# Kernel tuning notes

Hardware: AMD Instinct MI355X
Metric: run time of the kernel (lower is better)

Reference implementation:

```python
import jax, jax.numpy as jnp
import numpy as np

T, B = 256, 512
IMG_FLAT = 25          # 5*5*num_channels
FEAT = 16; LOC = 4; EMB = 4
LSTM_IN = FEAT + LOC + EMB  # 24
H = 128
GRID = 10.0


def _lin(k, out_d, in_d, scale=0.05):
    kw, kb = jax.random.split(k)
    return (jax.random.normal(kw, (out_d, in_d), jnp.float32) * scale,
            jax.random.normal(kb, (out_d,), jnp.float32) * scale)


def setup_inputs() -> dict:
    key = jax.random.key(0)
    ks = jax.random.split(key, 16)
    image = jax.random.uniform(ks[0], (T * B, 5, 5), jnp.float32) * 255.0
    location = jax.random.uniform(ks[1], (T * B, 2), jnp.float32) * GRID
    message = jax.random.normal(ks[2], (T * B, 1), jnp.float32)
    done = jax.random.randint(ks[3], (T * B,), 0, 2, jnp.int32)
    h0 = jnp.zeros((1, B, H), jnp.float32)
    c0 = jnp.zeros((1, B, H), jnp.float32)
    Wv1, bv1 = _lin(ks[4], 256, IMG_FLAT)
    Wv2, bv2 = _lin(ks[5], 256, 256)
    Wv3, bv3 = _lin(ks[6], 128, 256)
    Wv4, bv4 = _lin(ks[7], FEAT, 128)
    Wl, bl = _lin(ks[8], LOC, 2)
    Wm, bm = _lin(ks[9], EMB, 1)
    Wih, bih = _lin(ks[10], 4 * H, LSTM_IN)
    Whh, bhh = _lin(ks[11], 4 * H, H)
    return dict(image=image, location=location, message=message, done=done,
                h0=h0, c0=c0,
                Wv1=Wv1, bv1=bv1, Wv2=Wv2, bv2=bv2, Wv3=Wv3, bv3=bv3,
                Wv4=Wv4, bv4=bv4, Wl=Wl, bl=bl, Wm=Wm, bm=bm,
                Wih=Wih, bih=bih, Whh=Whh, bhh=bhh)


def _get_states(image, location, message, done_f, h0, c0,
                Wv1, bv1, Wv2, bv2, Wv3, bv3, Wv4, bv4,
                Wl, bl, Wm, bm, Wih, bih, Whh, bhh):
    batch = h0.shape[1]
    # encoders (all rows at once, faithful to torch version)
    x = image.reshape(image.shape[0], -1) / 255.0
    f = jax.nn.relu(x @ Wv1.T + bv1)
    f = jax.nn.relu(f @ Wv2.T + bv2)
    f = jax.nn.relu(f @ Wv3.T + bv3)
    image_feat = jax.nn.relu(f @ Wv4.T + bv4)                  # [TB, 16]
    loc_feat = (location / GRID) @ Wl.T + bl                    # [TB, 4]
    msg = (1.0 - done_f)[:, None] * message
    msg_feat = jax.nn.relu(msg @ Wm.T + bm)                     # [TB, 4]
    hid = jnp.concatenate([image_feat, loc_feat, msg_feat], axis=1)
    hid = hid.reshape(-1, batch, LSTM_IN)                       # [T, B, 24]
    d_seq = done_f.reshape(-1, batch)                           # [T, B]

    def step(carry, xd):
        h, c = carry
        x_t, d_t = xd
        mask = (1.0 - d_t)[:, None]
        h = h * mask
        c = c * mask
        gates = x_t @ Wih.T + bih + h @ Whh.T + bhh             # [B, 4H]
        i, fg, g, o = jnp.split(gates, 4, axis=-1)
        c = jax.nn.sigmoid(fg) * c + jax.nn.sigmoid(i) * jnp.tanh(g)
        h = jax.nn.sigmoid(o) * jnp.tanh(c)
        return (h, c), h

    (hT, cT), hs = jax.lax.scan(step, (h0[0], c0[0]), (hid, d_seq))
    new_hidden = hs.reshape(-1, H)                              # [TB, 128]
    return new_hidden, hT[None], cT[None]


def reference(image, location, message, done, h0, c0,
              Wv1, bv1, Wv2, bv2, Wv3, bv3, Wv4, bv4,
              Wl, bl, Wm, bm, Wih, bih, Whh, bhh):
    done_f = done.astype(jnp.float32)
    return _get_states(image, location, message, done_f, h0, c0,
                       Wv1, bv1, Wv2, bv2, Wv3, bv3, Wv4, bv4,
                       Wl, bl, Wm, bm, Wih, bih, Whh, bhh)
```

## Files before the change

kernel.cpp:

```cpp
#include <hip/hip_runtime.h>
#include <hip/hip_bf16.h>

#define T_STEPS 256
#define BATCH   512
#define HID     128
#define TBROWS  (T_STEPS * BATCH)
#define XH_STRIDE 32

typedef short  bh8   __attribute__((ext_vector_type(8)));
typedef _Float16 h8  __attribute__((ext_vector_type(8)));
typedef float  f32x4 __attribute__((ext_vector_type(4)));

__device__ __forceinline__ unsigned short f2bf_bits(float x) {
    union { float f; unsigned int u; } a; a.f = x;
    unsigned int r = a.u + 0x7fffu + ((a.u >> 16) & 1u);
    return (unsigned short)(r >> 16);
}
__device__ __forceinline__ unsigned short f2h_bits(float x) {
    union { _Float16 h; unsigned short u; } z; z.h = (_Float16)x; return z.u;
}
__device__ __forceinline__ unsigned int pack2h(float a, float b) {
    union { _Float16 h[2]; unsigned int u; } z;
    z.h[0] = (_Float16)a; z.h[1] = (_Float16)b; return z.u;
}
__device__ __forceinline__ unsigned int pack2bf(float a, float b) {
    return (unsigned int)f2bf_bits(a) | ((unsigned int)f2bf_bits(b) << 16);
}

#if __has_builtin(__builtin_amdgcn_rcpf)
__device__ __forceinline__ float frcp(float x) { return __builtin_amdgcn_rcpf(x); }
#else
__device__ __forceinline__ float frcp(float x) { return 1.0f / x; }
#endif
#if __has_builtin(__builtin_amdgcn_exp2f)
__device__ __forceinline__ float fexp2(float x) { return __builtin_amdgcn_exp2f(x); }
#else
__device__ __forceinline__ float fexp2(float x) { return __expf(x * 0.6931471806f); }
#endif
#define LOG2E 1.442695041f
__device__ __forceinline__ float sigf(float x) {
    return frcp(1.0f + fexp2(-x * LOG2E));
}
__device__ __forceinline__ float tanh_fast(float x) {
    return fmaf(-2.0f, frcp(1.0f + fexp2(x * (2.0f * LOG2E))), 1.0f);
}

__device__ __forceinline__ float swz16(float v) {
    return __int_as_float(
        __builtin_amdgcn_ds_swizzle(__float_as_int(v), 0x000F));
}

__device__ __forceinline__ void barrier_lds_only() {
    asm volatile("s_waitcnt lgkmcnt(0)" ::: "memory");
    __builtin_amdgcn_s_barrier();
    asm volatile("" ::: "memory");
}

__device__ __forceinline__ void fragstore(unsigned short* dst, const float* W,
                                          int i, int NT, int Kreal) {
    const int j    = i & 7;
    const int lane = (i >> 3) & 63;
    const int ts   = i >> 9;
    const int nt   = ts % NT;
    const int ks   = ts / NT;
    const int n = nt * 16 + (lane & 15);
    const int k = ks * 32 + (lane >> 4) * 8 + j;
    dst[i] = (k < Kreal) ? f2bf_bits(W[n * Kreal + k]) : (unsigned short)0;
}

#define NE1 8192
#define NE2 65536
#define NE3 32768
#define NE4 2048
#define NWC 81920
#define NBS 512
#define PREP_TOTAL (NE1 + NE2 + NE3 + NE4 + NWC + NBS)

__global__ __launch_bounds__(256) void prep_kernel(
    const float* __restrict__ W1, const float* __restrict__ W2,
    const float* __restrict__ W3, const float* __restrict__ W4,
    const float* __restrict__ Wih, const float* __restrict__ bih,
    const float* __restrict__ Whh, const float* __restrict__ bhh,
    unsigned short* __restrict__ w1f, unsigned short* __restrict__ w2f,
    unsigned short* __restrict__ w3f, unsigned short* __restrict__ w4f,
    unsigned short* __restrict__ wcf, float* __restrict__ bsum)
{
    int i = blockIdx.x * 256 + threadIdx.x;
    if (i < NE1) { fragstore(w1f, W1, i, 16, 25); return; }
    i -= NE1;
    if (i < NE2) { fragstore(w2f, W2, i, 16, 256); return; }
    i -= NE2;
    if (i < NE3) { fragstore(w3f, W3, i, 8, 256); return; }
    i -= NE3;
    if (i < NE4) { fragstore(w4f, W4, i, 1, 128); return; }
    i -= NE4;
    if (i < NWC) {
        const int j    = i & 7;
        const int lane = (i >> 3) & 63;
        const int ts   = i >> 9;
        const int mt   = ts / 5;
        const int kt   = ts - mt * 5;
        const int m = mt * 16 + (lane & 15);
        const int k = kt * 32 + (lane >> 4) * 8 + j;
        float v = 0.0f;
        if (k < 128)      v = Whh[m * 128 + k];
        else if (k < 152) v = Wih[m * 24 + (k - 128)];
        wcf[i] = f2h_bits(v);
        return;
    }
    i -= NWC;
    if (i < NBS) bsum[i] = bih[i] + bhh[i];
}

#define ASTRIDE 264

__global__ __launch_bounds__(256) void encoder_kernel(
    const float* __restrict__ img,
    const float* __restrict__ loc,
    const float* __restrict__ msg,
    const int*   __restrict__ done,
    const float* __restrict__ B1, const float* __restrict__ B2,
    const float* __restrict__ B3, const float* __restrict__ B4,
    const float* __restrict__ Wl, const float* __restrict__ Bl,
    const float* __restrict__ Wm, const float* __restrict__ Bm,
    const unsigned short* __restrict__ w1f, const unsigned short* __restrict__ w2f,
    const unsigned short* __restrict__ w3f, const unsigned short* __restrict__ w4f,
    unsigned short* __restrict__ xcat_h)
{
    __shared__ __align__(16) unsigned short actA[4][32][ASTRIDE];
    __shared__ __align__(16) unsigned short actB[4][32][ASTRIDE];

    const int tid  = threadIdx.x;
    const int w    = tid >> 6;
    const int lane = tid & 63;
    const int n    = lane & 15;
    const int quad = lane >> 4;
    const int wrow0 = blockIdx.x * 128 + w * 32;

    if (tid < 128) {
        const int grow = blockIdx.x * 128 + tid;
        const float l0 = loc[(size_t)grow * 2 + 0] * 0.1f;
        const float l1 = loc[(size_t)grow * 2 + 1] * 0.1f;
        #pragma unroll
        for (int c = 0; c < 4; ++c)
            xcat_h[(size_t)grow * XH_STRIDE + 16 + c] =
                f2h_bits(fmaf(Wl[c * 2 + 0], l0, fmaf(Wl[c * 2 + 1], l1, Bl[c])));
        const float mm = (1.0f - (float)done[grow]) * msg[grow];
        #pragma unroll
        for (int c = 0; c < 4; ++c)
            xcat_h[(size_t)grow * XH_STRIDE + 20 + c] =
                f2h_bits(fmaxf(fmaf(Wm[c], mm, Bm[c]), 0.0f));
    }

    const f32x4 zero4 = {0.0f, 0.0f, 0.0f, 0.0f};

    {
        bh8 bimg[2];
        #pragma unroll
        for (int sg = 0; sg < 2; ++sg) {
            const size_t grow = wrow0 + sg * 16 + n;
            #pragma unroll
            for (int j = 0; j < 8; ++j) {
                const int k = quad * 8 + j;
                const float v = (k < 25) ? img[grow * 25 + k] * (1.0f / 255.0f) : 0.0f;
                bimg[sg][j] = (short)f2bf_bits(v);
            }
        }
        f32x4 a1[16][2];
        #pragma unroll
        for (int mt = 0; mt < 16; ++mt) {
            const bh8 a = *reinterpret_cast<const bh8*>(w1f + (size_t)(mt * 64 + lane) * 8);
            a1[mt][0] = __builtin_amdgcn_mfma_f32_16x16x32_bf16(a, bimg[0], zero4, 0, 0, 0);
            a1[mt][1] = __builtin_amdgcn_mfma_f32_16x16x32_bf16(a, bimg[1], zero4, 0, 0, 0);
        }
        #pragma unroll
        for (int mt = 0; mt < 16; ++mt) {
            const float4 bv = *reinterpret_cast<const float4*>(B1 + mt * 16 + quad * 4);
            #pragma unroll
            for (int sg = 0; sg < 2; ++sg) {
                const float v0 = fmaxf(a1[mt][sg][0] + bv.x, 0.0f);
                const float v1 = fmaxf(a1[mt][sg][1] + bv.y, 0.0f);
                const float v2 = fmaxf(a1[mt][sg][2] + bv.z, 0.0f);
                const float v3 = fmaxf(a1[mt][sg][3] + bv.w, 0.0f);
                uint2 pk; pk.x = pack2bf(v0, v1); pk.y = pack2bf(v2, v3);
                *reinterpret_cast<uint2*>(&actA[w][sg * 16 + n][mt * 16 + quad * 4]) = pk;
            }
        }
    }
    __syncthreads();

    {
        f32x4 a2[16][2];
        #pragma unroll
        for (int mt = 0; mt < 16; ++mt) { a2[mt][0] = zero4; a2[mt][1] = zero4; }
        #pragma unroll
        for (int kt = 0; kt < 8; ++kt) {
            const bh8 b0 = *reinterpret_cast<const bh8*>(&actA[w][n][kt * 32 + quad * 8]);
            const bh8 b1 = *reinterpret_cast<const bh8*>(&actA[w][16 + n][kt * 32 + quad * 8]);
            #pragma unroll
            for (int mt = 0; mt < 16; ++mt) {
                const bh8 a = *reinterpret_cast<const bh8*>(
                    w2f + (size_t)((kt * 16 + mt) * 64 + lane) * 8);
                a2[mt][0] = __builtin_amdgcn_mfma_f32_16x16x32_bf16(a, b0, a2[mt][0], 0, 0, 0);
                a2[mt][1] = __builtin_amdgcn_mfma_f32_16x16x32_bf16(a, b1, a2[mt][1], 0, 0, 0);
            }
        }
        #pragma unroll
        for (int mt = 0; mt < 16; ++mt) {
            const float4 bv = *reinterpret_cast<const float4*>(B2 + mt * 16 + quad * 4);
            #pragma unroll
            for (int sg = 0; sg < 2; ++sg) {
                const float v0 = fmaxf(a2[mt][sg][0] + bv.x, 0.0f);
                const float v1 = fmaxf(a2[mt][sg][1] + bv.y, 0.0f);
                const float v2 = fmaxf(a2[mt][sg][2] + bv.z, 0.0f);
                const float v3 = fmaxf(a2[mt][sg][3] + bv.w, 0.0f);
                uint2 pk; pk.x = pack2bf(v0, v1); pk.y = pack2bf(v2, v3);
                *reinterpret_cast<uint2*>(&actB[w][sg * 16 + n][mt * 16 + quad * 4]) = pk;
            }
        }
    }
    __syncthreads();

    {
        f32x4 a3[8][2];
        #pragma unroll
        for (int mt = 0; mt < 8; ++mt) { a3[mt][0] = zero4; a3[mt][1] = zero4; }
        #pragma unroll
        for (int kt = 0; kt < 8; ++kt) {
            const bh8 b0 = *reinterpret_cast<const bh8*>(&actB[w][n][kt * 32 + quad * 8]);
            const bh8 b1 = *reinterpret_cast<const bh8*>(&actB[w][16 + n][kt * 32 + quad * 8]);
            #pragma unroll
            for (int mt = 0; mt < 8; ++mt) {
                const bh8 a = *reinterpret_cast<const bh8*>(
                    w3f + (size_t)((kt * 8 + mt) * 64 + lane) * 8);
                a3[mt][0] = __builtin_amdgcn_mfma_f32_16x16x32_bf16(a, b0, a3[mt][0], 0, 0, 0);
                a3[mt][1] = __builtin_amdgcn_mfma_f32_16x16x32_bf16(a, b1, a3[mt][1], 0, 0, 0);
            }
        }
        #pragma unroll
        for (int mt = 0; mt < 8; ++mt) {
            const float4 bv = *reinterpret_cast<const float4*>(B3 + mt * 16 + quad * 4);
            #pragma unroll
            for (int sg = 0; sg < 2; ++sg) {
                const float v0 = fmaxf(a3[mt][sg][0] + bv.x, 0.0f);
                const float v1 = fmaxf(a3[mt][sg][1] + bv.y, 0.0f);
                const float v2 = fmaxf(a3[mt][sg][2] + bv.z, 0.0f);
                const float v3 = fmaxf(a3[mt][sg][3] + bv.w, 0.0f);
                uint2 pk; pk.x = pack2bf(v0, v1); pk.y = pack2bf(v2, v3);
                *reinterpret_cast<uint2*>(&actA[w][sg * 16 + n][mt * 16 + quad * 4]) = pk;
            }
        }
    }
    __syncthreads();

    {
        f32x4 a4[2] = {zero4, zero4};
        #pragma unroll
        for (int kt = 0; kt < 4; ++kt) {
            const bh8 b0 = *reinterpret_cast<const bh8*>(&actA[w][n][kt * 32 + quad * 8]);
            const bh8 b1 = *reinterpret_cast<const bh8*>(&actA[w][16 + n][kt * 32 + quad * 8]);
            const bh8 a = *reinterpret_cast<const bh8*>(w4f + (size_t)(kt * 64 + lane) * 8);
            a4[0] = __builtin_amdgcn_mfma_f32_16x16x32_bf16(a, b0, a4[0], 0, 0, 0);
            a4[1] = __builtin_amdgcn_mfma_f32_16x16x32_bf16(a, b1, a4[1], 0, 0, 0);
        }
        const float4 bv = *reinterpret_cast<const float4*>(B4 + quad * 4);
        #pragma unroll
        for (int sg = 0; sg < 2; ++sg) {
            const int grow = wrow0 + sg * 16 + n;
            const float v0 = fmaxf(a4[sg][0] + bv.x, 0.0f);
            const float v1 = fmaxf(a4[sg][1] + bv.y, 0.0f);
            const float v2 = fmaxf(a4[sg][2] + bv.z, 0.0f);
            const float v3 = fmaxf(a4[sg][3] + bv.w, 0.0f);
            uint2 pk; pk.x = pack2h(v0, v1); pk.y = pack2h(v2, v3);
            *reinterpret_cast<uint2*>(xcat_h + (size_t)grow * XH_STRIDE + quad * 4) = pk;
        }
    }
}

#define COLS 2

__global__ __launch_bounds__(512) void lstm_kernel(
    const unsigned short* __restrict__ xcat_h,
    const int*   __restrict__ done,
    const float* __restrict__ h0,
    const float* __restrict__ c0,
    const unsigned short* __restrict__ wcf,
    const float* __restrict__ bsum,
    float* __restrict__ out)
{
    __shared__ __align__(16) unsigned short xls[T_STEPS][COLS][32];
    __shared__ __align__(16) unsigned short hx[2][COLS][HID];
    __shared__ int dls[T_STEPS][COLS];

    const int tid  = threadIdx.x;
    const int w    = tid >> 6;
    const int lane = tid & 63;
    const int n    = lane & 15;
    const int quad = lane >> 4;
    const int bb   = blockIdx.x * COLS;

    for (int i = tid; i < T_STEPS * COLS * 16; i += 512) {
        const int dw = i & 15;
        const int rc = i >> 4;
        const int st = rc >> 1, cl = rc & 1;
        unsigned int v = 0u;
        if (dw < 12)
            v = *reinterpret_cast<const unsigned int*>(
                xcat_h + (size_t)(st * BATCH + bb + cl) * XH_STRIDE + dw * 2);
        *reinterpret_cast<unsigned int*>(&xls[st][cl][dw * 2]) = v;
    }
    if (tid < T_STEPS * COLS) {
        const int st = tid >> 1, cl = tid & 1;
        dls[st][cl] = done[st * BATCH + bb + cl];
    }

    h8 wf[4][5];
    #pragma unroll
    for (int g = 0; g < 4; ++g)
        #pragma unroll
        for (int kt = 0; kt < 5; ++kt)
            wf[g][kt] = *reinterpret_cast<const h8*>(
                wcf + (size_t)(((g * 8 + w) * 5 + kt) * 64 + lane) * 8);

    const int unit = w * 16 + n;
    f32x4 bini[4];
    #pragma unroll
    for (int g = 0; g < 4; ++g) {
        const float b = bsum[g * 128 + unit];
        bini[g] = (f32x4){b, b, b, b};
    }

    const bool owner = (lane < 32);
    const int col = quad & 1;

    float c_ = 0.0f, h0v = 0.0f;
    if (owner) {
        c_  = c0[(size_t)(bb + col) * HID + unit];
        h0v = h0[(size_t)(bb + col) * HID + unit];
    }
    __syncthreads();

    if (owner)
        hx[0][col][unit] = f2h_bits(h0v * (1.0f - (float)dls[0][col]));
    __syncthreads();

    float hl = 0.0f;

    h8 bf[5];
    #pragma unroll
    for (int kt = 0; kt < 5; ++kt) bf[kt] = (h8)(_Float16)0.0f;

    #pragma unroll 1
    for (int s = 0; s < T_STEPS; ++s) {
        const int buf = s & 1;

        if (n < COLS) {
            #pragma unroll
            for (int kt = 0; kt < 4; ++kt)
                bf[kt] = *reinterpret_cast<const h8*>(&hx[buf][n][kt * 32 + quad * 8]);
            bf[4] = *reinterpret_cast<const h8*>(&xls[s][n][quad * 8]);
        }

        const int sn = (s + 1 < T_STEPS) ? s + 1 : T_STEPS - 1;
        const int m_cur = dls[s][col];
        const int m_nxt = dls[sn][col];

        f32x4 acc[4];
        #pragma unroll
        for (int g = 0; g < 4; ++g) acc[g] = bini[g];
        #pragma unroll
        for (int kt = 0; kt < 5; ++kt)
            #pragma unroll
            for (int g = 0; g < 4; ++g)
                acc[g] = __builtin_amdgcn_mfma_f32_16x16x32_f16(
                    bf[kt], wf[g][kt], acc[g], 0, 0, 0);

        float g4[4];
        #pragma unroll
        for (int g = 0; g < 4; ++g) {
            const float t0 = swz16(acc[g][0]);
            const float t1 = swz16(acc[g][1]);
            g4[g] = (lane & 16) ? t1 : t0;
        }

        if (owner) {
            const float cn = sigf(g4[1]) * (c_ * (1.0f - (float)m_cur))
                           + sigf(g4[0]) * tanh_fast(g4[2]);
            const float hn = sigf(g4[3]) * tanh_fast(cn);
            c_ = cn; hl = hn;
            out[(size_t)(s * BATCH + bb + col) * HID + unit] = hn;
            hx[buf ^ 1][col][unit] = f2h_bits(hn * (1.0f - (float)m_nxt));
        }
        barrier_lds_only();
    }

    const size_t base = (size_t)TBROWS * HID;
    if (owner) {
        out[base + (size_t)(bb + col) * HID + unit] = hl;
        out[base + (size_t)BATCH * HID + (size_t)(bb + col) * HID + unit] = c_;
    }
}

extern "C" void kernel_launch(void* const* d_in, const int* in_sizes, int n_in,
                              void* d_out, int out_size, void* d_ws, size_t ws_size,
                              hipStream_t stream) {
    const float* img  = (const float*)d_in[0];
    const float* loc  = (const float*)d_in[1];
    const float* msg  = (const float*)d_in[2];
    const int*   done = (const int*)d_in[3];
    const float* h0   = (const float*)d_in[4];
    const float* c0   = (const float*)d_in[5];
    const float* W1   = (const float*)d_in[6];
    const float* B1   = (const float*)d_in[7];
    const float* W2   = (const float*)d_in[8];
    const float* B2   = (const float*)d_in[9];
    const float* W3   = (const float*)d_in[10];
    const float* B3   = (const float*)d_in[11];
    const float* W4   = (const float*)d_in[12];
    const float* B4   = (const float*)d_in[13];
    const float* Wl   = (const float*)d_in[14];
    const float* Bl   = (const float*)d_in[15];
    const float* Wm   = (const float*)d_in[16];
    const float* Bm   = (const float*)d_in[17];
    const float* Wih  = (const float*)d_in[18];
    const float* bih  = (const float*)d_in[19];
    const float* Whh  = (const float*)d_in[20];
    const float* bhh  = (const float*)d_in[21];

    char* wsb = (char*)d_ws;
    unsigned short* xcat_h = (unsigned short*)wsb;
    unsigned short* w1f = (unsigned short*)(wsb + (size_t)TBROWS * XH_STRIDE * 2);
    unsigned short* w2f = w1f + NE1;
    unsigned short* w3f = w2f + NE2;
    unsigned short* w4f = w3f + NE3;
    unsigned short* wcf = w4f + NE4;
    float*          bsum = (float*)(wcf + NWC);

    float* out = (float*)d_out;

    prep_kernel<<<(PREP_TOTAL + 255) / 256, 256, 0, stream>>>(
        W1, W2, W3, W4, Wih, bih, Whh, bhh,
        w1f, w2f, w3f, w4f, wcf, bsum);
    encoder_kernel<<<TBROWS / 128, 256, 0, stream>>>(
        img, loc, msg, done, B1, B2, B3, B4, Wl, Bl, Wm, Bm,
        w1f, w2f, w3f, w4f, xcat_h);
    lstm_kernel<<<BATCH / COLS, 512, 0, stream>>>(
        xcat_h, done, h0, c0, wcf, bsum, out);
}
```

Before: 378.1 us.

## Assign one batch column per LSTM block and drop cross-lane swizzle

```diff
diff --git a/kernel.cpp b/kernel.cpp
--- a/kernel.cpp
+++ b/kernel.cpp
@@ -43,11 +43,6 @@
 }
 __device__ __forceinline__ float tanh_fast(float x) {
     return fmaf(-2.0f, frcp(1.0f + fexp2(x * (2.0f * LOG2E))), 1.0f);
-}
-
-__device__ __forceinline__ float swz16(float v) {
-    return __int_as_float(
-        __builtin_amdgcn_ds_swizzle(__float_as_int(v), 0x000F));
 }
 
 __device__ __forceinline__ void barrier_lds_only() {
@@ -277,9 +272,7 @@
     }
 }
 
-#define COLS 2
-
-__global__ __launch_bounds__(512) void lstm_kernel(
+__global__ __launch_bounds__(512, 4) void lstm_kernel(
     const unsigned short* __restrict__ xcat_h,
     const int*   __restrict__ done,
     const float* __restrict__ h0,
@@ -288,31 +281,27 @@
     const float* __restrict__ bsum,
     float* __restrict__ out)
 {
-    __shared__ __align__(16) unsigned short xls[T_STEPS][COLS][32];
-    __shared__ __align__(16) unsigned short hx[2][COLS][HID];
-    __shared__ int dls[T_STEPS][COLS];
+    __shared__ __align__(16) unsigned short xls[T_STEPS][32];
+    __shared__ __align__(16) unsigned short hx[2][HID];
+    __shared__ int dls[T_STEPS];
 
     const int tid  = threadIdx.x;
     const int w    = tid >> 6;
     const int lane = tid & 63;
     const int n    = lane & 15;
     const int quad = lane >> 4;
-    const int bb   = blockIdx.x * COLS;
-
-    for (int i = tid; i < T_STEPS * COLS * 16; i += 512) {
+    const int b    = blockIdx.x;
+
+    for (int i = tid; i < T_STEPS * 16; i += 512) {
         const int dw = i & 15;
-        const int rc = i >> 4;
-        const int st = rc >> 1, cl = rc & 1;
+        const int st = i >> 4;
         unsigned int v = 0u;
         if (dw < 12)
             v = *reinterpret_cast<const unsigned int*>(
-                xcat_h + (size_t)(st * BATCH + bb + cl) * XH_STRIDE + dw * 2);
-        *reinterpret_cast<unsigned int*>(&xls[st][cl][dw * 2]) = v;
-    }
-    if (tid < T_STEPS * COLS) {
-        const int st = tid >> 1, cl = tid & 1;
-        dls[st][cl] = done[st * BATCH + bb + cl];
-    }
+                xcat_h + (size_t)(st * BATCH + b) * XH_STRIDE + dw * 2);
+        *reinterpret_cast<unsigned int*>(&xls[st][dw * 2]) = v;
+    }
+    if (tid < T_STEPS) dls[tid] = done[tid * BATCH + b];
 
     h8 wf[4][5];
     #pragma unroll
@@ -326,22 +315,21 @@
     f32x4 bini[4];
     #pragma unroll
     for (int g = 0; g < 4; ++g) {
-        const float b = bsum[g * 128 + unit];
-        bini[g] = (f32x4){b, b, b, b};
-    }
-
-    const bool owner = (lane < 32);
-    const int col = quad & 1;
+        const float bv = bsum[g * 128 + unit];
+        bini[g] = (f32x4){bv, bv, bv, bv};
+    }
+
+    const bool owner = (quad == 0);
 
     float c_ = 0.0f, h0v = 0.0f;
     if (owner) {
-        c_  = c0[(size_t)(bb + col) * HID + unit];
-        h0v = h0[(size_t)(bb + col) * HID + unit];
+        c_  = c0[(size_t)b * HID + unit];
+        h0v = h0[(size_t)b * HID + unit];
     }
     __syncthreads();
 
     if (owner)
-        hx[0][col][unit] = f2h_bits(h0v * (1.0f - (float)dls[0][col]));
+        hx[0][unit] = f2h_bits(h0v * (1.0f - (float)dls[0]));
     __syncthreads();
 
     float hl = 0.0f;
@@ -354,16 +342,16 @@
     for (int s = 0; s < T_STEPS; ++s) {
         const int buf = s & 1;
 
-        if (n < COLS) {
+        if (n == 0) {
             #pragma unroll
             for (int kt = 0; kt < 4; ++kt)
-                bf[kt] = *reinterpret_cast<const h8*>(&hx[buf][n][kt * 32 + quad * 8]);
-            bf[4] = *reinterpret_cast<const h8*>(&xls[s][n][quad * 8]);
+                bf[kt] = *reinterpret_cast<const h8*>(&hx[buf][kt * 32 + quad * 8]);
+            bf[4] = *reinterpret_cast<const h8*>(&xls[s][quad * 8]);
         }
 
         const int sn = (s + 1 < T_STEPS) ? s + 1 : T_STEPS - 1;
-        const int m_cur = dls[s][col];
-        const int m_nxt = dls[sn][col];
+        const int m_cur = dls[s];
+        const int m_nxt = dls[sn];
 
         f32x4 acc[4];
         #pragma unroll
@@ -375,29 +363,21 @@
                 acc[g] = __builtin_amdgcn_mfma_f32_16x16x32_f16(
                     bf[kt], wf[g][kt], acc[g], 0, 0, 0);
 
-        float g4[4];
-        #pragma unroll
-        for (int g = 0; g < 4; ++g) {
-            const float t0 = swz16(acc[g][0]);
-            const float t1 = swz16(acc[g][1]);
-            g4[g] = (lane & 16) ? t1 : t0;
-        }
-
         if (owner) {
-            const float cn = sigf(g4[1]) * (c_ * (1.0f - (float)m_cur))
-                           + sigf(g4[0]) * tanh_fast(g4[2]);
-            const float hn = sigf(g4[3]) * tanh_fast(cn);
+            const float cn = sigf(acc[1][0]) * (c_ * (1.0f - (float)m_cur))
+                           + sigf(acc[0][0]) * tanh_fast(acc[2][0]);
+            const float hn = sigf(acc[3][0]) * tanh_fast(cn);
             c_ = cn; hl = hn;
-            out[(size_t)(s * BATCH + bb + col) * HID + unit] = hn;
-            hx[buf ^ 1][col][unit] = f2h_bits(hn * (1.0f - (float)m_nxt));
+            out[(size_t)(s * BATCH + b) * HID + unit] = hn;
+            hx[buf ^ 1][unit] = f2h_bits(hn * (1.0f - (float)m_nxt));
         }
         barrier_lds_only();
     }
 
     const size_t base = (size_t)TBROWS * HID;
     if (owner) {
-        out[base + (size_t)(bb + col) * HID + unit] = hl;
-        out[base + (size_t)BATCH * HID + (size_t)(bb + col) * HID + unit] = c_;
+        out[base + (size_t)b * HID + unit] = hl;
+        out[base + (size_t)BATCH * HID + (size_t)b * HID + unit] = c_;
     }
 }
 
@@ -444,6 +424,6 @@
     encoder_kernel<<<TBROWS / 128, 256, 0, stream>>>(
         img, loc, msg, done, B1, B2, B3, B4, Wl, Bl, Wm, Bm,
         w1f, w2f, w3f, w4f, xcat_h);
-    lstm_kernel<<<BATCH / COLS, 512, 0, stream>>>(
+    lstm_kernel<<<BATCH, 512, 0, stream>>>(
         xcat_h, done, h0, c0, wcf, bsum, out);
 }
```

After: 763.8 us. 2.02x slower.

## Split encoder output features across waves sharing one 64-row block

Applied to the files above, without the earlier changes.

```diff
diff --git a/kernel.cpp b/kernel.cpp
--- a/kernel.cpp
+++ b/kernel.cpp
@@ -113,6 +113,7 @@
 }
 
 #define ASTRIDE 264
+#define ESAMP 64
 
 __global__ __launch_bounds__(256) void encoder_kernel(
     const float* __restrict__ img,
@@ -127,18 +128,18 @@
     const unsigned short* __restrict__ w3f, const unsigned short* __restrict__ w4f,
     unsigned short* __restrict__ xcat_h)
 {
-    __shared__ __align__(16) unsigned short actA[4][32][ASTRIDE];
-    __shared__ __align__(16) unsigned short actB[4][32][ASTRIDE];
+    __shared__ __align__(16) unsigned short actA[ESAMP][ASTRIDE];
+    __shared__ __align__(16) unsigned short actB[ESAMP][ASTRIDE];
 
     const int tid  = threadIdx.x;
     const int w    = tid >> 6;
     const int lane = tid & 63;
     const int n    = lane & 15;
     const int quad = lane >> 4;
-    const int wrow0 = blockIdx.x * 128 + w * 32;
-
-    if (tid < 128) {
-        const int grow = blockIdx.x * 128 + tid;
+    const int row0 = blockIdx.x * ESAMP;
+
+    if (tid < ESAMP) {
+        const int grow = row0 + tid;
         const float l0 = loc[(size_t)grow * 2 + 0] * 0.1f;
         const float l1 = loc[(size_t)grow * 2 + 1] * 0.1f;
         #pragma unroll
@@ -155,10 +156,10 @@
     const f32x4 zero4 = {0.0f, 0.0f, 0.0f, 0.0f};
 
     {
-        bh8 bimg[2];
-        #pragma unroll
-        for (int sg = 0; sg < 2; ++sg) {
-            const size_t grow = wrow0 + sg * 16 + n;
+        bh8 bimg[4];
+        #pragma unroll
+        for (int sg = 0; sg < 4; ++sg) {
+            const size_t grow = row0 + sg * 16 + n;
             #pragma unroll
             for (int j = 0; j < 8; ++j) {
                 const int k = quad * 8 + j;
@@ -166,114 +167,122 @@
                 bimg[sg][j] = (short)f2bf_bits(v);
             }
         }
-        f32x4 a1[16][2];
-        #pragma unroll
-        for (int mt = 0; mt < 16; ++mt) {
-            const bh8 a = *reinterpret_cast<const bh8*>(w1f + (size_t)(mt * 64 + lane) * 8);
-            a1[mt][0] = __builtin_amdgcn_mfma_f32_16x16x32_bf16(a, bimg[0], zero4, 0, 0, 0);
-            a1[mt][1] = __builtin_amdgcn_mfma_f32_16x16x32_bf16(a, bimg[1], zero4, 0, 0, 0);
-        }
-        #pragma unroll
-        for (int mt = 0; mt < 16; ++mt) {
-            const float4 bv = *reinterpret_cast<const float4*>(B1 + mt * 16 + quad * 4);
-            #pragma unroll
-            for (int sg = 0; sg < 2; ++sg) {
-                const float v0 = fmaxf(a1[mt][sg][0] + bv.x, 0.0f);
-                const float v1 = fmaxf(a1[mt][sg][1] + bv.y, 0.0f);
-                const float v2 = fmaxf(a1[mt][sg][2] + bv.z, 0.0f);
-                const float v3 = fmaxf(a1[mt][sg][3] + bv.w, 0.0f);
+        #pragma unroll
+        for (int mt = 0; mt < 4; ++mt) {
+            const int mtg = w * 4 + mt;
+            const bh8 a = *reinterpret_cast<const bh8*>(w1f + (size_t)(mtg * 64 + lane) * 8);
+            f32x4 acc[4];
+            #pragma unroll
+            for (int sg = 0; sg < 4; ++sg)
+                acc[sg] = __builtin_amdgcn_mfma_f32_16x16x32_bf16(a, bimg[sg], zero4, 0, 0, 0);
+            const float4 bv = *reinterpret_cast<const float4*>(B1 + mtg * 16 + quad * 4);
+            #pragma unroll
+            for (int sg = 0; sg < 4; ++sg) {
+                const float v0 = fmaxf(acc[sg][0] + bv.x, 0.0f);
+                const float v1 = fmaxf(acc[sg][1] + bv.y, 0.0f);
+                const float v2 = fmaxf(acc[sg][2] + bv.z, 0.0f);
+                const float v3 = fmaxf(acc[sg][3] + bv.w, 0.0f);
                 uint2 pk; pk.x = pack2bf(v0, v1); pk.y = pack2bf(v2, v3);
-                *reinterpret_cast<uint2*>(&actA[w][sg * 16 + n][mt * 16 + quad * 4]) = pk;
+                *reinterpret_cast<uint2*>(&actA[sg * 16 + n][mtg * 16 + quad * 4]) = pk;
             }
         }
     }
     __syncthreads();
 
     {
-        f32x4 a2[16][2];
-        #pragma unroll
-        for (int mt = 0; mt < 16; ++mt) { a2[mt][0] = zero4; a2[mt][1] = zero4; }
+        f32x4 a2[4][4];
+        #pragma unroll
+        for (int mt = 0; mt < 4; ++mt)
+            #pragma unroll
+            for (int sg = 0; sg < 4; ++sg) a2[mt][sg] = zero4;
         #pragma unroll
         for (int kt = 0; kt < 8; ++kt) {
-            const bh8 b0 = *reinterpret_cast<const bh8*>(&actA[w][n][kt * 32 + quad * 8]);
-            const bh8 b1 = *reinterpret_cast<const bh8*>(&actA[w][16 + n][kt * 32 + quad * 8]);
-            #pragma unroll
-            for (int mt = 0; mt < 16; ++mt) {
+            bh8 b[4];
+            #pragma unroll
+            for (int sg = 0; sg < 4; ++sg)
+                b[sg] = *reinterpret_cast<const bh8*>(&actA[sg * 16 + n][kt * 32 + quad * 8]);
+            #pragma unroll
+            for (int mt = 0; mt < 4; ++mt) {
+                const int mtg = w * 4 + mt;
                 const bh8 a = *reinterpret_cast<const bh8*>(
-                    w2f + (size_t)((kt * 16 + mt) * 64 + lane) * 8);
-                a2[mt][0] = __builtin_amdgcn_mfma_f32_16x16x32_bf16(a, b0, a2[mt][0], 0, 0, 0);
-                a2[mt][1] = __builtin_amdgcn_mfma_f32_16x16x32_bf16(a, b1, a2[mt][1], 0, 0, 0);
-            }
-        }
-        #pragma unroll
-        for (int mt = 0; mt < 16; ++mt) {
-            const float4 bv = *reinterpret_cast<const float4*>(B2 + mt * 16 + quad * 4);
-            #pragma unroll
-            for (int sg = 0; sg < 2; ++sg) {
+                    w2f + (size_t)((kt * 16 + mtg) * 64 + lane) * 8);
+                #pragma unroll
+                for (int sg = 0; sg < 4; ++sg)
+                    a2[mt][sg] = __builtin_amdgcn_mfma_f32_16x16x32_bf16(a, b[sg], a2[mt][sg], 0, 0, 0);
+            }
+        }
+        #pragma unroll
+        for (int mt = 0; mt < 4; ++mt) {
+            const int mtg = w * 4 + mt;
+            const float4 bv = *reinterpret_cast<const float4*>(B2 + mtg * 16 + quad * 4);
+            #pragma unroll
+            for (int sg = 0; sg < 4; ++sg) {
                 const float v0 = fmaxf(a2[mt][sg][0] + bv.x, 0.0f);
                 const float v1 = fmaxf(a2[mt][sg][1] + bv.y, 0.0f);
                 const float v2 = fmaxf(a2[mt][sg][2] + bv.z, 0.0f);
                 const float v3 = fmaxf(a2[mt][sg][3] + bv.w, 0.0f);
                 uint2 pk; pk.x = pack2bf(v0, v1); pk.y = pack2bf(v2, v3);
-                *reinterpret_cast<uint2*>(&actB[w][sg * 16 + n][mt * 16 + quad * 4]) = pk;
+                *reinterpret_cast<uint2*>(&actB[sg * 16 + n][mtg * 16 + quad * 4]) = pk;
             }
         }
     }
     __syncthreads();
 
     {
-        f32x4 a3[8][2];
-        #pragma unroll
-        for (int mt = 0; mt < 8; ++mt) { a3[mt][0] = zero4; a3[mt][1] = zero4; }
+        f32x4 a3[2][4];
+        #pragma unroll
+        for (int mt = 0; mt < 2; ++mt)
+            #pragma unroll
+            for (int sg = 0; sg < 4; ++sg) a3[mt][sg] = zero4;
         #pragma unroll
         for (int kt = 0; kt < 8; ++kt) {
-            const bh8 b0 = *reinterpret_cast<const bh8*>(&actB[w][n][kt * 32 + quad * 8]);
-            const bh8 b1 = *reinterpret_cast<const bh8*>(&actB[w][16 + n][kt * 32 + quad * 8]);
-            #pragma unroll
-            for (int mt = 0; mt < 8; ++mt) {
+            bh8 b[4];
+            #pragma unroll
+            for (int sg = 0; sg < 4; ++sg)
+                b[sg] = *reinterpret_cast<const bh8*>(&actB[sg * 16 + n][kt * 32 + quad * 8]);
+            #pragma unroll
+            for (int mt = 0; mt < 2; ++mt) {
+                const int mtg = w * 2 + mt;
                 const bh8 a = *reinterpret_cast<const bh8*>(
-                    w3f + (size_t)((kt * 8 + mt) * 64 + lane) * 8);
-                a3[mt][0] = __builtin_amdgcn_mfma_f32_16x16x32_bf16(a, b0, a3[mt][0], 0, 0, 0);
-                a3[mt][1] = __builtin_amdgcn_mfma_f32_16x16x32_bf16(a, b1, a3[mt][1], 0, 0, 0);
-            }
-        }
-        #pragma unroll
-        for (int mt = 0; mt < 8; ++mt) {
-            const float4 bv = *reinterpret_cast<const float4*>(B3 + mt * 16 + quad * 4);
-            #pragma unroll
-            for (int sg = 0; sg < 2; ++sg) {
+                    w3f + (size_t)((kt * 8 + mtg) * 64 + lane) * 8);
+                #pragma unroll
+                for (int sg = 0; sg < 4; ++sg)
+                    a3[mt][sg] = __builtin_amdgcn_mfma_f32_16x16x32_bf16(a, b[sg], a3[mt][sg], 0, 0, 0);
+            }
+        }
+        #pragma unroll
+        for (int mt = 0; mt < 2; ++mt) {
+            const int mtg = w * 2 + mt;
+            const float4 bv = *reinterpret_cast<const float4*>(B3 + mtg * 16 + quad * 4);
+            #pragma unroll
+            for (int sg = 0; sg < 4; ++sg) {
                 const float v0 = fmaxf(a3[mt][sg][0] + bv.x, 0.0f);
                 const float v1 = fmaxf(a3[mt][sg][1] + bv.y, 0.0f);
                 const float v2 = fmaxf(a3[mt][sg][2] + bv.z, 0.0f);
                 const float v3 = fmaxf(a3[mt][sg][3] + bv.w, 0.0f);
                 uint2 pk; pk.x = pack2bf(v0, v1); pk.y = pack2bf(v2, v3);
-                *reinterpret_cast<uint2*>(&actA[w][sg * 16 + n][mt * 16 + quad * 4]) = pk;
+                *reinterpret_cast<uint2*>(&actA[sg * 16 + n][mtg * 16 + quad * 4]) = pk;
             }
         }
     }
     __syncthreads();
 
     {
-        f32x4 a4[2] = {zero4, zero4};
+        f32x4 a4 = zero4;
         #pragma unroll
         for (int kt = 0; kt < 4; ++kt) {
-            const bh8 b0 = *reinterpret_cast<const bh8*>(&actA[w][n][kt * 32 + quad * 8]);
-            const bh8 b1 = *reinterpret_cast<const bh8*>(&actA[w][16 + n][kt * 32 + quad * 8]);
+            const bh8 b = *reinterpret_cast<const bh8*>(&actA[w * 16 + n][kt * 32 + quad * 8]);
             const bh8 a = *reinterpret_cast<const bh8*>(w4f + (size_t)(kt * 64 + lane) * 8);
-            a4[0] = __builtin_amdgcn_mfma_f32_16x16x32_bf16(a, b0, a4[0], 0, 0, 0);
-            a4[1] = __builtin_amdgcn_mfma_f32_16x16x32_bf16(a, b1, a4[1], 0, 0, 0);
+            a4 = __builtin_amdgcn_mfma_f32_16x16x32_bf16(a, b, a4, 0, 0, 0);
         }
         const float4 bv = *reinterpret_cast<const float4*>(B4 + quad * 4);
-        #pragma unroll
-        for (int sg = 0; sg < 2; ++sg) {
-            const int grow = wrow0 + sg * 16 + n;
-            const float v0 = fmaxf(a4[sg][0] + bv.x, 0.0f);
-            const float v1 = fmaxf(a4[sg][1] + bv.y, 0.0f);
-            const float v2 = fmaxf(a4[sg][2] + bv.z, 0.0f);
-            const float v3 = fmaxf(a4[sg][3] + bv.w, 0.0f);
-            uint2 pk; pk.x = pack2h(v0, v1); pk.y = pack2h(v2, v3);
-            *reinterpret_cast<uint2*>(xcat_h + (size_t)grow * XH_STRIDE + quad * 4) = pk;
-        }
+        const int grow = row0 + w * 16 + n;
+        const float v0 = fmaxf(a4[0] + bv.x, 0.0f);
+        const float v1 = fmaxf(a4[1] + bv.y, 0.0f);
+        const float v2 = fmaxf(a4[2] + bv.z, 0.0f);
+        const float v3 = fmaxf(a4[3] + bv.w, 0.0f);
+        uint2 pk; pk.x = pack2h(v0, v1); pk.y = pack2h(v2, v3);
+        *reinterpret_cast<uint2*>(xcat_h + (size_t)grow * XH_STRIDE + quad * 4) = pk;
     }
 }
 
@@ -441,7 +450,7 @@
     prep_kernel<<<(PREP_TOTAL + 255) / 256, 256, 0, stream>>>(
         W1, W2, W3, W4, Wih, bih, Whh, bhh,
         w1f, w2f, w3f, w4f, wcf, bsum);
-    encoder_kernel<<<TBROWS / 128, 256, 0, stream>>>(
+    encoder_kernel<<<TBROWS / ESAMP, 256, 0, stream>>>(
         img, loc, msg, done, B1, B2, B3, B4, Wl, Bl, Wm, Bm,
         w1f, w2f, w3f, w4f, xcat_h);
     lstm_kernel<<<BATCH / COLS, 512, 0, stream>>>(
```

New measurement: 344.4 us. -8.9%, faster.
